# Kernel optimization log

Hardware: AMD Instinct MI355X
Metric: run time of the kernel (lower is better)

## Reference

```python
import jax, jax.numpy as jnp
import numpy as np

B = 4096       # batch size
DIM = 1024     # feature dim
E = 9          # 8 session experts + 1 default layer (index 8)


def setup_inputs() -> dict:
    key = jax.random.key(0)
    k_x, k_w, k_b, k_i = jax.random.split(key, 4)
    x = jax.random.normal(k_x, (B, DIM), dtype=jnp.float32)
    # Stacked nn.Linear params: W[e] has torch layout [out, in], b[e] is [out].
    # (Original init is identity+zero bias; random values exercise the same math.)
    W = jax.random.normal(k_w, (E, DIM, DIM), dtype=jnp.float32) * (DIM ** -0.5)
    b = jax.random.normal(k_b, (E, DIM), dtype=jnp.float32)
    session_idx = jax.random.randint(k_i, (B,), 0, E, dtype=jnp.int64)
    return {"x": x, "W": W, "b": b, "session_idx": session_idx}


def reference(x, W, b, session_idx):
    # Per-sample keyed linear: out[i] = x[i] @ W[session_idx[i]].T + b[session_idx[i]].
    # Dense formulation: run every expert on every sample (E small), then select.
    # y: [B, E, DIM]
    y = jnp.einsum('bd,eod->beo', x, W) + b[None, :, :]
    out = y[jnp.arange(x.shape[0]), session_idx]  # [B, DIM]
    return out
```

## Files before the change

kernel.cpp:

```cpp
#include <hip/hip_runtime.h>
#include <hip/hip_bf16.h>

#define NE 9
#define NDIM 1024
#define BM 128
#define BN 128
#define BK 64
#define NT (NDIM / BK)
#define NSLOT_MAX 48
#define SPX (NSLOT_MAX / 8)

typedef __attribute__((ext_vector_type(8))) short bf16x8;
typedef __attribute__((ext_vector_type(4))) float f32x4;

__device__ __forceinline__ unsigned pack2_bf16(float a, float b) {
    __hip_bfloat162 h = __float22bfloat162_rn(float2{a, b});
    return *reinterpret_cast<unsigned*>(&h);
}

__device__ __forceinline__ void gload_lds16(const void* g, void* l) {
    __builtin_amdgcn_global_load_lds(
        (const __attribute__((address_space(1))) unsigned int*)g,
        (__attribute__((address_space(3))) unsigned int*)l, 16, 0, 0);
}

__global__ __launch_bounds__(256)
void prep_kernel(const float* __restrict__ x, const float* __restrict__ W,
                 const int* __restrict__ sidx,
                 unsigned short* __restrict__ xb, unsigned short* __restrict__ Wb,
                 int* __restrict__ perm, int4* __restrict__ desc, int nB) {
    if (blockIdx.x == 0) {
        __shared__ int cnt[NE];
        __shared__ int cur[NE];
        int t = threadIdx.x;
        if (t < NE) cnt[t] = 0;
        __syncthreads();
        for (int i = t; i < nB; i += 256) atomicAdd(&cnt[sidx[i]], 1);
        __syncthreads();
        if (t == 0) {
            int run = 0, s = 0;
            for (int e = 0; e < NE; ++e) {
                cur[e] = run;
                int c = cnt[e];
                for (int m0 = 0; m0 < c; m0 += BM) {
                    desc[s] = make_int4(e, run + m0, min(BM, c - m0), 0);
                    ++s;
                }
                run += c;
            }
            for (; s < NSLOT_MAX; ++s) desc[s] = make_int4(-1, 0, 1, 0);
        }
        __syncthreads();
        for (int i = t; i < nB; i += 256) {
            int p = atomicAdd(&cur[sidx[i]], 1);
            perm[p] = i;
        }
    } else {
        const int NW8 = NE * NDIM * (NDIM / 8);
        const int NX8 = nB * (NDIM / 8);
        const int tot = NW8 + NX8;
        const int stride = (gridDim.x - 1) * 256;
        for (int u = (blockIdx.x - 1) * 256 + threadIdx.x; u < tot; u += stride) {
            const float4* src;
            uint4* dst;
            if (u < NW8) {
                src = (const float4*)W + 2 * (size_t)u;
                dst = (uint4*)Wb + u;
            } else {
                size_t v = (size_t)(u - NW8);
                src = (const float4*)x + 2 * v;
                dst = (uint4*)xb + v;
            }
            float4 a = src[0], c = src[1];
            uint4 o;
            o.x = pack2_bf16(a.x, a.y);
            o.y = pack2_bf16(a.z, a.w);
            o.z = pack2_bf16(c.x, c.y);
            o.w = pack2_bf16(c.z, c.w);
            *dst = o;
        }
    }
}

__global__ __launch_bounds__(256, 2)
void gemm_kernel(const unsigned short* __restrict__ xb,
                 const unsigned short* __restrict__ Wb,
                 const float* __restrict__ bias,
                 const int* __restrict__ perm,
                 const int4* __restrict__ desc,
                 float* __restrict__ out) {
    const int b    = blockIdx.x;
    const int xcd  = b & 7;
    const int loc  = b >> 3;
    const int slot = xcd * SPX + (loc >> 3);
    const int n    = loc & 7;
    const int4 d   = desc[slot];
    if (d.x < 0) return;
    const int e = d.x, rowstart = d.y, rcnt = d.z;
    const int n0 = n * BN;

    __shared__ __align__(16) unsigned short lds[32768];

    const int t    = threadIdx.x;
    const int wave = t >> 6;
    const int lane = t & 63;
    const int fr   = lane & 15;
    const int fq   = lane >> 4;
    const int wr   = (wave >> 1) * 64;
    const int wc   = (wave & 1) * 64;
    const int xr   = fr & 7;

    const int srow = t >> 3;
    const int scol = ((t & 7) ^ (srow & 7)) * 8;

    const unsigned short* asrc[4];
#pragma unroll
    for (int i = 0; i < 4; ++i) {
        int lm = i * 32 + srow;
        if (lm >= rcnt) lm = rcnt - 1;
        asrc[i] = xb + (size_t)perm[rowstart + lm] * NDIM + scol;
    }
    const unsigned short* bsrc = Wb + ((size_t)e * NDIM + n0 + srow) * NDIM + scol;

#define STAGE(BUF, K0)                                                         \
    do {                                                                       \
        _Pragma("unroll")                                                      \
        for (int i = 0; i < 4; ++i) {                                          \
            gload_lds16(asrc[i] + (K0),                                        \
                        &lds[(BUF) * 8192 + i * 2048 + wave * 512]);           \
            gload_lds16(bsrc + (size_t)i * 32 * NDIM + (K0),                   \
                        &lds[16384 + (BUF) * 8192 + i * 2048 + wave * 512]);   \
        }                                                                      \
    } while (0)

    f32x4 acc[4][4];
#pragma unroll
    for (int i = 0; i < 4; ++i)
#pragma unroll
        for (int k = 0; k < 4; ++k) acc[i][k] = (f32x4)(0.0f);

    STAGE(0, 0);
    __syncthreads();

    for (int tt = 0; tt < NT; ++tt) {
        const int cur = tt & 1;
        if (tt + 1 < NT) STAGE(cur ^ 1, (tt + 1) * BK);

        const int abase = cur * 8192;
        const int bbase = 16384 + cur * 8192;
#pragma unroll
        for (int kk = 0; kk < 2; ++kk) {
            const int cs = ((kk * 4 + fq) ^ xr) * 8;
            bf16x8 af[4], bfv[4];
#pragma unroll
            for (int mf = 0; mf < 4; ++mf)
                af[mf] = *reinterpret_cast<const bf16x8*>(
                    &lds[abase + (wr + mf * 16 + fr) * 64 + cs]);
#pragma unroll
            for (int nf = 0; nf < 4; ++nf)
                bfv[nf] = *reinterpret_cast<const bf16x8*>(
                    &lds[bbase + (wc + nf * 16 + fr) * 64 + cs]);
#pragma unroll
            for (int mf = 0; mf < 4; ++mf)
#pragma unroll
                for (int nf = 0; nf < 4; ++nf)
                    acc[mf][nf] = __builtin_amdgcn_mfma_f32_16x16x32_bf16(
                        af[mf], bfv[nf], acc[mf][nf], 0, 0, 0);
        }
        __syncthreads();
    }
#undef STAGE

    float bl[4];
#pragma unroll
    for (int nf = 0; nf < 4; ++nf)
        bl[nf] = bias[e * NDIM + n0 + wc + nf * 16 + fr];

#pragma unroll
    for (int mf = 0; mf < 4; ++mf) {
#pragma unroll
        for (int jr = 0; jr < 4; ++jr) {
            int lm = wr + mf * 16 + fq * 4 + jr;
            if (lm < rcnt) {
                int grow = perm[rowstart + lm];
                float* orow = out + (size_t)grow * NDIM;
#pragma unroll
                for (int nf = 0; nf < 4; ++nf)
                    orow[n0 + wc + nf * 16 + fr] = acc[mf][nf][jr] + bl[nf];
            }
        }
    }
}

__global__ void naive_kernel(const float* __restrict__ x, const float* __restrict__ W,
                             const float* __restrict__ bias,
                             const int* __restrict__ sidx, float* __restrict__ out,
                             int nB) {
    int i = blockIdx.x;
    int c = threadIdx.x + (blockIdx.y << 8);
    if (i >= nB || c >= NDIM) return;
    int e = sidx[i];
    const float* wrow = W + ((size_t)e * NDIM + c) * NDIM;
    const float* xr = x + (size_t)i * NDIM;
    float s = bias[e * NDIM + c];
    for (int k = 0; k < NDIM; ++k) s += xr[k] * wrow[k];
    out[(size_t)i * NDIM + c] = s;
}

extern "C" void kernel_launch(void* const* d_in, const int* in_sizes, int n_in,
                              void* d_out, int out_size, void* d_ws, size_t ws_size,
                              hipStream_t stream) {
    const float* x    = (const float*)d_in[0];
    const float* W    = (const float*)d_in[1];
    const float* bias = (const float*)d_in[2];
    const int*   sidx = (const int*)d_in[3];
    float*       out  = (float*)d_out;

    const int nB = in_sizes[3];

    char* wsb = (char*)d_ws;
    size_t p_desc = (size_t)nB * 4;
    size_t p_xb   = ((p_desc + NSLOT_MAX * 16 + 511) / 512) * 512;
    size_t p_wb   = p_xb + (size_t)nB * NDIM * 2;
    size_t need   = p_wb + (size_t)NE * NDIM * NDIM * 2;

    if (ws_size < need) {
        dim3 g(nB, NDIM / 256);
        naive_kernel<<<g, 256, 0, stream>>>(x, W, bias, sidx, out, nB);
        return;
    }

    int*  perm = (int*)wsb;
    int4* desc = (int4*)(wsb + p_desc);
    unsigned short* xb = (unsigned short*)(wsb + p_xb);
    unsigned short* Wb = (unsigned short*)(wsb + p_wb);

    prep_kernel<<<1024, 256, 0, stream>>>(x, W, sidx, xb, Wb, perm, desc, nB);

    gemm_kernel<<<NSLOT_MAX * 8, 256, 0, stream>>>(xb, Wb, bias, perm, desc, out);
}
```

Baseline: 44.03 us.

## Split GEMM K dimension in two with atomic accumulation over bias-initialized output

Splits the K reduction of each tile across two workgroups, doubling the grid so more CUs are busy given only about 40 row-tile slots times 8 column tiles. The output is first filled with the per-row bias by a new kernel, and each half then accumulates its partial sums with float atomicAdd. This adds an extra full pass writing the output, atomic read-modify-write traffic on the output, and an additional kernel launch.

New measurement: 71.14 us. 61.6% more time.

```diff
diff --git a/kernel.cpp b/kernel.cpp
--- a/kernel.cpp
+++ b/kernel.cpp
@@ -6,7 +6,9 @@
 #define BM 128
 #define BN 128
 #define BK 64
-#define NT (NDIM / BK)
+#define KSPLIT 2
+#define KHALF (NDIM / KSPLIT)
+#define NTH (KHALF / BK)
 #define NSLOT_MAX 48
 #define SPX (NSLOT_MAX / 8)
 
@@ -82,22 +84,38 @@
     }
 }
 
+__global__ __launch_bounds__(256)
+void bias_init_kernel(const float* __restrict__ bias, const int* __restrict__ sidx,
+                      float* __restrict__ out, int nB) {
+    const int tot = nB * (NDIM / 4);
+    const int stride = gridDim.x * blockDim.x;
+    for (int u = blockIdx.x * blockDim.x + threadIdx.x; u < tot; u += stride) {
+        int row = u >> 8;
+        int c4 = u & 255;
+        int e = sidx[row];
+        ((float4*)out)[u] =
+            ((const float4*)(bias + (size_t)e * NDIM))[c4];
+    }
+}
+
 __global__ __launch_bounds__(256, 2)
 void gemm_kernel(const unsigned short* __restrict__ xb,
                  const unsigned short* __restrict__ Wb,
-                 const float* __restrict__ bias,
                  const int* __restrict__ perm,
                  const int4* __restrict__ desc,
                  float* __restrict__ out) {
     const int b    = blockIdx.x;
     const int xcd  = b & 7;
     const int loc  = b >> 3;
-    const int slot = xcd * SPX + (loc >> 3);
-    const int n    = loc & 7;
+    const int slot = xcd * SPX + (loc >> 4);
+    const int rem  = loc & 15;
+    const int n    = rem >> 1;
+    const int kh   = rem & 1;
     const int4 d   = desc[slot];
     if (d.x < 0) return;
     const int e = d.x, rowstart = d.y, rcnt = d.z;
     const int n0 = n * BN;
+    const int k0base = kh * KHALF;
 
     __shared__ __align__(16) unsigned short lds[32768];
 
@@ -118,9 +136,10 @@
     for (int i = 0; i < 4; ++i) {
         int lm = i * 32 + srow;
         if (lm >= rcnt) lm = rcnt - 1;
-        asrc[i] = xb + (size_t)perm[rowstart + lm] * NDIM + scol;
-    }
-    const unsigned short* bsrc = Wb + ((size_t)e * NDIM + n0 + srow) * NDIM + scol;
+        asrc[i] = xb + (size_t)perm[rowstart + lm] * NDIM + k0base + scol;
+    }
+    const unsigned short* bsrc =
+        Wb + ((size_t)e * NDIM + n0 + srow) * NDIM + k0base + scol;
 
 #define STAGE(BUF, K0)                                                         \
     do {                                                                       \
@@ -142,9 +161,9 @@
     STAGE(0, 0);
     __syncthreads();
 
-    for (int tt = 0; tt < NT; ++tt) {
+    for (int tt = 0; tt < NTH; ++tt) {
         const int cur = tt & 1;
-        if (tt + 1 < NT) STAGE(cur ^ 1, (tt + 1) * BK);
+        if (tt + 1 < NTH) STAGE(cur ^ 1, (tt + 1) * BK);
 
         const int abase = cur * 8192;
         const int bbase = 16384 + cur * 8192;
@@ -170,11 +189,6 @@
         __syncthreads();
     }
 #undef STAGE
-
-    float bl[4];
-#pragma unroll
-    for (int nf = 0; nf < 4; ++nf)
-        bl[nf] = bias[e * NDIM + n0 + wc + nf * 16 + fr];
 
 #pragma unroll
     for (int mf = 0; mf < 4; ++mf) {
@@ -186,7 +200,7 @@
                 float* orow = out + (size_t)grow * NDIM;
 #pragma unroll
                 for (int nf = 0; nf < 4; ++nf)
-                    orow[n0 + wc + nf * 16 + fr] = acc[mf][nf][jr] + bl[nf];
+                    atomicAdd(&orow[n0 + wc + nf * 16 + fr], acc[mf][nf][jr]);
             }
         }
     }
@@ -236,6 +250,7 @@
     unsigned short* Wb = (unsigned short*)(wsb + p_wb);
 
     prep_kernel<<<1024, 256, 0, stream>>>(x, W, sidx, xb, Wb, perm, desc, nB);
-
-    gemm_kernel<<<NSLOT_MAX * 8, 256, 0, stream>>>(xb, Wb, bias, perm, desc, out);
-}
+    bias_init_kernel<<<2048, 256, 0, stream>>>(bias, sidx, out, nB);
+
+    gemm_kernel<<<NSLOT_MAX * 16, 256, 0, stream>>>(xb, Wb, perm, desc, out);
+}
```

## Fuse x bf16 conversion into GEMM A-tile load and halve row tile

Applied to the files above, without the earlier changes.

Removes the separate fp32-to-bf16 conversion pass over x from the prep kernel. The GEMM now loads fp32 x rows directly into LDS and packs them to bf16 when reading fragments. BM drops from 128 to 64 and the slot count rises to 80, which gives more, smaller tiles and less padding waste per expert. The cost is double the LDS footprint (64KB), twice the A-tile global traffic in fp32, conversion work inside the inner loop, and lower MFMA reuse per tile.

Result: slower. 59.49 us (+35.1%).

```diff
diff --git a/kernel.cpp b/kernel.cpp
--- a/kernel.cpp
+++ b/kernel.cpp
@@ -3,12 +3,11 @@
 
 #define NE 9
 #define NDIM 1024
-#define BM 128
+#define BM 64
 #define BN 128
 #define BK 64
 #define NT (NDIM / BK)
-#define NSLOT_MAX 48
-#define SPX (NSLOT_MAX / 8)
+#define NSLOT_MAX 80
 
 typedef __attribute__((ext_vector_type(8))) short bf16x8;
 typedef __attribute__((ext_vector_type(4))) float f32x4;
@@ -25,9 +24,8 @@
 }
 
 __global__ __launch_bounds__(256)
-void prep_kernel(const float* __restrict__ x, const float* __restrict__ W,
-                 const int* __restrict__ sidx,
-                 unsigned short* __restrict__ xb, unsigned short* __restrict__ Wb,
+void prep_kernel(const float* __restrict__ W, const int* __restrict__ sidx,
+                 unsigned short* __restrict__ Wb,
                  int* __restrict__ perm, int4* __restrict__ desc, int nB) {
     if (blockIdx.x == 0) {
         __shared__ int cnt[NE];
@@ -57,33 +55,22 @@
         }
     } else {
         const int NW8 = NE * NDIM * (NDIM / 8);
-        const int NX8 = nB * (NDIM / 8);
-        const int tot = NW8 + NX8;
         const int stride = (gridDim.x - 1) * 256;
-        for (int u = (blockIdx.x - 1) * 256 + threadIdx.x; u < tot; u += stride) {
-            const float4* src;
-            uint4* dst;
-            if (u < NW8) {
-                src = (const float4*)W + 2 * (size_t)u;
-                dst = (uint4*)Wb + u;
-            } else {
-                size_t v = (size_t)(u - NW8);
-                src = (const float4*)x + 2 * v;
-                dst = (uint4*)xb + v;
-            }
+        for (int u = (blockIdx.x - 1) * 256 + threadIdx.x; u < NW8; u += stride) {
+            const float4* src = (const float4*)W + 2 * (size_t)u;
             float4 a = src[0], c = src[1];
             uint4 o;
             o.x = pack2_bf16(a.x, a.y);
             o.y = pack2_bf16(a.z, a.w);
             o.z = pack2_bf16(c.x, c.y);
             o.w = pack2_bf16(c.z, c.w);
-            *dst = o;
+            ((uint4*)Wb)[u] = o;
         }
     }
 }
 
 __global__ __launch_bounds__(256, 2)
-void gemm_kernel(const unsigned short* __restrict__ xb,
+void gemm_kernel(const float* __restrict__ x,
                  const unsigned short* __restrict__ Wb,
                  const float* __restrict__ bias,
                  const int* __restrict__ perm,
@@ -91,51 +78,54 @@
                  float* __restrict__ out) {
     const int b    = blockIdx.x;
     const int xcd  = b & 7;
-    const int loc  = b >> 3;
-    const int slot = xcd * SPX + (loc >> 3);
-    const int n    = loc & 7;
+    const int j    = b >> 3;
+    const int slot = xcd * 10 + (j >> 3);
+    const int n    = j & 7;
     const int4 d   = desc[slot];
     if (d.x < 0) return;
     const int e = d.x, rowstart = d.y, rcnt = d.z;
     const int n0 = n * BN;
 
-    __shared__ __align__(16) unsigned short lds[32768];
+    __shared__ __align__(16) unsigned char lds[65536];
 
     const int t    = threadIdx.x;
     const int wave = t >> 6;
     const int lane = t & 63;
     const int fr   = lane & 15;
     const int fq   = lane >> 4;
-    const int wr   = (wave >> 1) * 64;
+    const int wr   = (wave >> 1) * 32;
     const int wc   = (wave & 1) * 64;
-    const int xr   = fr & 7;
-
-    const int srow = t >> 3;
-    const int scol = ((t & 7) ^ (srow & 7)) * 8;
-
-    const unsigned short* asrc[4];
+    const int xrB  = fr & 7;
+
+    const int arl  = t >> 4;
+    const int akey = (arl & 7) << 1;
+    const int aun  = (t & 15) ^ akey;
+    const float* ap[4];
 #pragma unroll
     for (int i = 0; i < 4; ++i) {
-        int lm = i * 32 + srow;
+        int lm = i * 16 + arl;
         if (lm >= rcnt) lm = rcnt - 1;
-        asrc[i] = xb + (size_t)perm[rowstart + lm] * NDIM + scol;
-    }
-    const unsigned short* bsrc = Wb + ((size_t)e * NDIM + n0 + srow) * NDIM + scol;
+        ap[i] = x + (size_t)perm[rowstart + lm] * NDIM + aun * 4;
+    }
+    const int brl  = t >> 3;
+    const unsigned short* bp =
+        Wb + ((size_t)e * NDIM + n0 + brl) * NDIM + ((t & 7) ^ (brl & 7)) * 8;
 
 #define STAGE(BUF, K0)                                                         \
     do {                                                                       \
         _Pragma("unroll")                                                      \
-        for (int i = 0; i < 4; ++i) {                                          \
-            gload_lds16(asrc[i] + (K0),                                        \
-                        &lds[(BUF) * 8192 + i * 2048 + wave * 512]);           \
-            gload_lds16(bsrc + (size_t)i * 32 * NDIM + (K0),                   \
-                        &lds[16384 + (BUF) * 8192 + i * 2048 + wave * 512]);   \
-        }                                                                      \
+        for (int i = 0; i < 4; ++i)                                            \
+            gload_lds16(ap[i] + (K0),                                          \
+                        &lds[(BUF) * 16384 + i * 4096 + wave * 1024]);         \
+        _Pragma("unroll")                                                      \
+        for (int i = 0; i < 4; ++i)                                            \
+            gload_lds16(bp + (size_t)i * 32 * NDIM + (K0),                     \
+                        &lds[32768 + (BUF) * 16384 + i * 4096 + wave * 1024]); \
     } while (0)
 
-    f32x4 acc[4][4];
-#pragma unroll
-    for (int i = 0; i < 4; ++i)
+    f32x4 acc[2][4];
+#pragma unroll
+    for (int i = 0; i < 2; ++i)
 #pragma unroll
         for (int k = 0; k < 4; ++k) acc[i][k] = (f32x4)(0.0f);
 
@@ -146,22 +136,34 @@
         const int cur = tt & 1;
         if (tt + 1 < NT) STAGE(cur ^ 1, (tt + 1) * BK);
 
-        const int abase = cur * 8192;
-        const int bbase = 16384 + cur * 8192;
+        const unsigned char* Ab = &lds[cur * 16384];
+        const unsigned char* Bb = &lds[32768 + cur * 16384];
 #pragma unroll
         for (int kk = 0; kk < 2; ++kk) {
-            const int cs = ((kk * 4 + fq) ^ xr) * 8;
-            bf16x8 af[4], bfv[4];
-#pragma unroll
-            for (int mf = 0; mf < 4; ++mf)
-                af[mf] = *reinterpret_cast<const bf16x8*>(
-                    &lds[abase + (wr + mf * 16 + fr) * 64 + cs]);
-#pragma unroll
-            for (int nf = 0; nf < 4; ++nf)
+            bf16x8 af[2], bfv[4];
+#pragma unroll
+            for (int mf = 0; mf < 2; ++mf) {
+                const int row = wr + mf * 16 + fr;
+                const int u   = (kk * 8 + fq * 2) ^ ((row & 7) << 1);
+                const float4* pa =
+                    reinterpret_cast<const float4*>(Ab + row * 256 + u * 16);
+                float4 lo = pa[0], hi = pa[1];
+                uint4 pk;
+                pk.x = pack2_bf16(lo.x, lo.y);
+                pk.y = pack2_bf16(lo.z, lo.w);
+                pk.z = pack2_bf16(hi.x, hi.y);
+                pk.w = pack2_bf16(hi.z, hi.w);
+                af[mf] = *reinterpret_cast<bf16x8*>(&pk);
+            }
+#pragma unroll
+            for (int nf = 0; nf < 4; ++nf) {
+                const int row = wc + nf * 16 + fr;
+                const int cs  = ((kk * 4 + fq) ^ xrB) * 8;
                 bfv[nf] = *reinterpret_cast<const bf16x8*>(
-                    &lds[bbase + (wc + nf * 16 + fr) * 64 + cs]);
-#pragma unroll
-            for (int mf = 0; mf < 4; ++mf)
+                    Bb + row * 128 + cs * 2);
+            }
+#pragma unroll
+            for (int mf = 0; mf < 2; ++mf)
 #pragma unroll
                 for (int nf = 0; nf < 4; ++nf)
                     acc[mf][nf] = __builtin_amdgcn_mfma_f32_16x16x32_bf16(
@@ -177,7 +179,7 @@
         bl[nf] = bias[e * NDIM + n0 + wc + nf * 16 + fr];
 
 #pragma unroll
-    for (int mf = 0; mf < 4; ++mf) {
+    for (int mf = 0; mf < 2; ++mf) {
 #pragma unroll
         for (int jr = 0; jr < 4; ++jr) {
             int lm = wr + mf * 16 + fq * 4 + jr;
@@ -220,8 +222,7 @@
 
     char* wsb = (char*)d_ws;
     size_t p_desc = (size_t)nB * 4;
-    size_t p_xb   = ((p_desc + NSLOT_MAX * 16 + 511) / 512) * 512;
-    size_t p_wb   = p_xb + (size_t)nB * NDIM * 2;
+    size_t p_wb   = ((p_desc + NSLOT_MAX * 16 + 511) / 512) * 512;
     size_t need   = p_wb + (size_t)NE * NDIM * NDIM * 2;
 
     if (ws_size < need) {
@@ -232,10 +233,9 @@
 
     int*  perm = (int*)wsb;
     int4* desc = (int4*)(wsb + p_desc);
-    unsigned short* xb = (unsigned short*)(wsb + p_xb);
     unsigned short* Wb = (unsigned short*)(wsb + p_wb);
 
-    prep_kernel<<<1024, 256, 0, stream>>>(x, W, sidx, xb, Wb, perm, desc, nB);
-
-    gemm_kernel<<<NSLOT_MAX * 8, 256, 0, stream>>>(xb, Wb, bias, perm, desc, out);
-}
+    prep_kernel<<<1024, 256, 0, stream>>>(W, sidx, Wb, perm, desc, nB);
+
+    gemm_kernel<<<NSLOT_MAX * 8, 256, 0, stream>>>(x, Wb, bias, perm, desc, out);
+}
```
